# Kernel optimization log

Measured on AMD Instinct MI355X. Metric: run time of the kernel, lower is better.

The kernel has to match this reference:

```python
import jax, jax.numpy as jnp
import numpy as np

jax.config.update("jax_enable_x64", True)  # torch casts to double for matrix_exp

EPS_DIAG = 1e-6


def setup_inputs() -> dict:
    key = jax.random.key(0)
    B, D, NB, S = 32, 128, 8, 128
    ks = jax.random.split(key, 9)
    return {
        "z0r": jax.random.normal(ks[0], (B, D), jnp.float32),
        "z0i": jax.random.normal(ks[1], (B, D), jnp.float32),
        # uniform grid: dt = time_steps[0] = 0.01, diffs == dt (uniform branch)
        "time_steps": (jnp.arange(S, dtype=jnp.float32) + 1.0) * 0.01,
        "k_coeffs": jax.random.normal(ks[2], (B, NB), jnp.float32),
        "r_coeffs": jax.random.normal(ks[3], (B, NB), jnp.float32),
        "alpha": jax.random.normal(ks[4], (B, 1), jnp.float32),
        "beta": jax.random.normal(ks[5], (B, 1), jnp.float32),
        "K_bases": jax.random.normal(ks[6], (NB, D, D), jnp.float32) * 0.01,
        "R_bases": jax.random.normal(ks[7], (NB, D, D), jnp.float32) * 0.01,
    }


def _build_generator(k_coeffs, r_coeffs, alpha, beta, K_bases, R_bases):
    # A = alpha * skew(K_sum) + beta * -(R_sum^T @ R_sum), per batch element
    K_sum = jnp.einsum("bn,nij->bij", k_coeffs, K_bases)
    R_sum = jnp.einsum("bn,nij->bij", r_coeffs, R_bases)
    skew = K_sum - jnp.swapaxes(K_sum, -1, -2)
    neg_gram = -jnp.einsum("bji,bjk->bik", R_sum, R_sum)  # -(R^T @ R)
    return alpha[..., None] * skew + beta[..., None] * neg_gram  # (B, D, D)


def _propagators(A, time_steps, uniform):
    D = A.shape[-1]
    S = time_steps.shape[0]
    if uniform:
        dt = time_steps[0]
        A64 = A.astype(jnp.float64) * dt.astype(jnp.float64) + EPS_DIAG * jnp.eye(D, dtype=jnp.float64)
        M = jax.vmap(jax.scipy.linalg.expm)(A64).astype(jnp.complex64)  # (B, D, D)
        # cumulative matrix powers M, M^2, ..., M^S via O(log S) associative scan
        Ms = jnp.broadcast_to(M[:, None], (M.shape[0], S, D, D))
        props = jax.lax.associative_scan(jnp.matmul, Ms, axis=1)
    else:
        A_t = A[:, None].astype(jnp.float64) * time_steps.astype(jnp.float64)[None, :, None, None]
        props = jax.vmap(jax.vmap(jax.scipy.linalg.expm))(A_t).astype(jnp.complex64)
    return props  # (B, S, D, D)


def reference(z0r, z0i, time_steps, k_coeffs, r_coeffs, alpha, beta, K_bases, R_bases):
    ts = np.asarray(time_steps)
    uniform = ts.shape[0] <= 1 or np.allclose(ts[1:] - ts[:-1], ts[0], atol=1e-6)
    A = _build_generator(k_coeffs, r_coeffs, alpha, beta, K_bases, R_bases)
    props = _propagators(A, time_steps, uniform)
    z = (z0r + 1j * z0i).astype(jnp.complex64)  # (B, D)
    # z_evolved[b, s, o] = sum_i z[b, i] * props[b, s, o, i]
    return jnp.einsum("bi,bsoi->bso", z, props)
```

## Files before the change

kernel.cpp:

```cpp
#include <hip/hip_runtime.h>

#define BATCH   32
#define DIM     128
#define NBASES  8
#define SSTEPS  128
#define LDA     136

typedef __attribute__((ext_vector_type(8))) short s8v;
typedef __attribute__((ext_vector_type(4))) short s4v;
typedef __attribute__((ext_vector_type(4))) float f4v;

__device__ __forceinline__ f4v mf(s8v a, s8v b, f4v c) {
    return __builtin_amdgcn_mfma_f32_16x16x32_bf16(a, b, c, 0, 0, 0);
}
__device__ __forceinline__ s8v ld8(const short* p) {
    return *reinterpret_cast<const s8v*>(p);
}
__device__ __forceinline__ s4v ld4(const short* p) {
    return *reinterpret_cast<const s4v*>(p);
}
__device__ __forceinline__ void st4(short* p, s4v v) {
    *reinterpret_cast<s4v*>(p) = v;
}
__device__ __forceinline__ float upbf(short h) {
    return __uint_as_float(((unsigned)(unsigned short)h) << 16);
}
__device__ __forceinline__ void splitbf(float v, short& hi, short& lo) {
    const unsigned u = __float_as_uint(v);
    hi = (short)(u >> 16);
    const float fh = __uint_as_float(u & 0xffff0000u);
    lo = (short)(__float_as_uint(v - fh) >> 16);
}

__device__ __forceinline__ void write_out(float* __restrict__ outF, int b, int sidx,
                                          int o, int c, float val,
                                          int interleaved, int out_size)
{
    if (interleaved) {
        const int oi = ((b * SSTEPS + sidx) * DIM + o) * 2 + c;
        if (oi < out_size) outF[oi] = val;
    } else if (c == 0) {
        const int oi = (b * SSTEPS + sidx) * DIM + o;
        if (oi < out_size) outF[oi] = val;
    }
}

template<bool DUAL>
__device__ __forceinline__ void mm_full(const short* __restrict__ Ah,
                                        const short* __restrict__ Al,
                                        const short* __restrict__ Bh,
                                        const short* __restrict__ Bl,
                                        f4v acc[2][2], f4v acct[2][2],
                                        int mb, int nb, int lane)
{
    const int l15 = lane & 15, quad = lane >> 4;
    #pragma unroll
    for (int kk = 0; kk < DIM; kk += 32) {
        const int ko = kk + quad * 8;
        s8v ah[2], al[2], bh[2], bl[2];
        #pragma unroll
        for (int i = 0; i < 2; ++i) {
            ah[i] = ld8(Ah + (mb + i * 16 + l15) * LDA + ko);
            al[i] = ld8(Al + (mb + i * 16 + l15) * LDA + ko);
            bh[i] = ld8(Bh + (nb + i * 16 + l15) * LDA + ko);
            bl[i] = ld8(Bl + (nb + i * 16 + l15) * LDA + ko);
        }
        #pragma unroll
        for (int mi = 0; mi < 2; ++mi)
            #pragma unroll
            for (int ni = 0; ni < 2; ++ni) {
                acc[mi][ni] = mf(ah[mi], bh[ni], acc[mi][ni]);
                acc[mi][ni] = mf(ah[mi], bl[ni], acc[mi][ni]);
                acc[mi][ni] = mf(al[mi], bh[ni], acc[mi][ni]);
                if (DUAL) {
                    acct[ni][mi] = mf(bh[ni], ah[mi], acct[ni][mi]);
                    acct[ni][mi] = mf(bl[ni], ah[mi], acct[ni][mi]);
                    acct[ni][mi] = mf(bh[ni], al[mi], acct[ni][mi]);
                }
            }
    }
}

__global__ __launch_bounds__(1024) __attribute__((amdgpu_waves_per_eu(4, 4)))
void htg_mfma(const float* __restrict__ z0r, const float* __restrict__ z0i,
              const float* __restrict__ ts,  const float* __restrict__ kco,
              const float* __restrict__ rco, const float* __restrict__ alp,
              const float* __restrict__ bet, const float* __restrict__ KB,
              const float* __restrict__ RB,  float* __restrict__ outF,
              int interleaved, int out_size)
{
    __shared__ short nm_hi[DIM * LDA], nm_lo[DIM * LDA];
    __shared__ short tr_hi[DIM * LDA], tr_lo[DIM * LDA];
    __shared__ short ht_hi[32 * LDA],  ht_lo[32 * LDA];
    float* s_part = reinterpret_cast<float*>(nm_hi);

    const int b = blockIdx.x, t = threadIdx.x;
    const int w = t >> 6, lane = t & 63;
    const int l15 = lane & 15, quad = lane >> 4;
    const f4v z4 = {0.f, 0.f, 0.f, 0.f};
    const int mb = (w & 3) * 32, nb = (w >> 2) * 32;

    {
        float rc[NBASES], kc[NBASES];
        #pragma unroll
        for (int n = 0; n < NBASES; ++n) {
            rc[n] = rco[b * NBASES + n];
            kc[n] = kco[b * NBASES + n];
        }
        #pragma unroll
        for (int q = 0; q < 4; ++q) {
            const int e = q * 4096 + t * 4;
            float4 r4 = {0.f, 0.f, 0.f, 0.f}, k4 = {0.f, 0.f, 0.f, 0.f};
            #pragma unroll
            for (int n = 0; n < NBASES; ++n) {
                const float4 rv = *reinterpret_cast<const float4*>(RB + n * DIM * DIM + e);
                const float4 kv = *reinterpret_cast<const float4*>(KB + n * DIM * DIM + e);
                r4.x += rc[n] * rv.x; r4.y += rc[n] * rv.y;
                r4.z += rc[n] * rv.z; r4.w += rc[n] * rv.w;
                k4.x += kc[n] * kv.x; k4.y += kc[n] * kv.y;
                k4.z += kc[n] * kv.z; k4.w += kc[n] * kv.w;
            }
            const int r = e >> 7, c = e & 127;
            const float rr[4] = {r4.x, r4.y, r4.z, r4.w};
            const float kk[4] = {k4.x, k4.y, k4.z, k4.w};
            s4v kh, kl;
            #pragma unroll
            for (int j = 0; j < 4; ++j) {
                short hi, lo;
                splitbf(rr[j], hi, lo);
                tr_hi[(c + j) * LDA + r] = hi; tr_lo[(c + j) * LDA + r] = lo;
                splitbf(kk[j], hi, lo);
                kh[j] = hi; kl[j] = lo;
            }
            st4(&nm_hi[r * LDA + c], kh);
            st4(&nm_lo[r * LDA + c], kl);
        }
        if (t < 2 * DIM) {
            const int c = t >> 7, o = t & 127;
            const float zv = (c == 0) ? z0r[b * DIM + o] : z0i[b * DIM + o];
            short hi, lo; splitbf(zv, hi, lo);
            ht_hi[c * LDA + o] = hi; ht_lo[c * LDA + o] = lo;
        }
    }
    __syncthreads();

    f4v acc[2][2], acct[2][2];
    float xsave[2][2][4];

    #pragma unroll
    for (int i = 0; i < 2; ++i)
        #pragma unroll
        for (int j = 0; j < 2; ++j) acc[i][j] = z4;
    mm_full<false>(tr_hi, tr_lo, tr_hi, tr_lo, acc, acct, mb, nb, lane);
    __syncthreads();
    {
        const float alpha = alp[b], beta = bet[b], dtf = ts[0];
        #pragma unroll
        for (int mi = 0; mi < 2; ++mi)
            #pragma unroll
            for (int ni = 0; ni < 2; ++ni) {
                const int row0 = mb + mi * 16 + quad * 4;
                const int col  = nb + ni * 16 + l15;
                const s4v k2h = ld4(&nm_hi[col * LDA + row0]);
                const s4v k2l = ld4(&nm_lo[col * LDA + row0]);
                #pragma unroll
                for (int r = 0; r < 4; ++r) {
                    const int row = row0 + r;
                    const float k1 = upbf(nm_hi[row * LDA + col]) + upbf(nm_lo[row * LDA + col]);
                    const float k2 = upbf(k2h[r]) + upbf(k2l[r]);
                    float x = (alpha * (k1 - k2) - beta * acc[mi][ni][r]) * dtf;
                    if (row == col) x += 1e-6f;
                    acc[mi][ni][r] = x;
                    xsave[mi][ni][r] = x;
                }
            }
    }
    __syncthreads();
    #pragma unroll
    for (int mi = 0; mi < 2; ++mi)
        #pragma unroll
        for (int ni = 0; ni < 2; ++ni) {
            const int row0 = mb + mi * 16 + quad * 4;
            const int col  = nb + ni * 16 + l15;
            s4v h4, l4;
            #pragma unroll
            for (int r = 0; r < 4; ++r) {
                short hi, lo;
                splitbf(acc[mi][ni][r], hi, lo);
                nm_hi[(row0 + r) * LDA + col] = hi;
                nm_lo[(row0 + r) * LDA + col] = lo;
                h4[r] = hi; l4[r] = lo;
            }
            st4(&tr_hi[col * LDA + row0], h4);
            st4(&tr_lo[col * LDA + row0], l4);
        }
    __syncthreads();

    #pragma unroll
    for (int i = 0; i < 2; ++i)
        #pragma unroll
        for (int j = 0; j < 2; ++j) { acc[i][j] = z4; acct[i][j] = z4; }
    mm_full<true>(nm_hi, nm_lo, tr_hi, tr_lo, acc, acct, mb, nb, lane);
    __syncthreads();
    #pragma unroll
    for (int mi = 0; mi < 2; ++mi)
        #pragma unroll
        for (int ni = 0; ni < 2; ++ni) {
            const int row0 = mb + mi * 16 + quad * 4;
            const int col  = nb + ni * 16 + l15;
            s4v h4, l4;
            #pragma unroll
            for (int r = 0; r < 4; ++r) {
                const int row = row0 + r;
                const float xv = xsave[mi][ni][r];
                const float cv = acc[mi][ni][r];
                const float a2 = xv * (1.f / 6.f) + cv * (1.f / 24.f);
                xsave[mi][ni][r] = ((row == col) ? 1.f : 0.f) + xv + 0.5f * cv;
                short hi, lo;
                splitbf(a2, hi, lo);
                h4[r] = hi; l4[r] = lo;
            }
            st4(&tr_hi[col * LDA + row0], h4);
            st4(&tr_lo[col * LDA + row0], l4);
        }
    #pragma unroll
    for (int ti = 0; ti < 2; ++ti)
        #pragma unroll
        for (int tj = 0; tj < 2; ++tj) {
            const int rt0 = nb + ti * 16 + quad * 4;
            const int ct  = mb + tj * 16 + l15;
            s4v h4, l4;
            #pragma unroll
            for (int r = 0; r < 4; ++r) {
                short hi, lo;
                splitbf(acct[ti][tj][r], hi, lo);
                h4[r] = hi; l4[r] = lo;
            }
            st4(&nm_hi[ct * LDA + rt0], h4);
            st4(&nm_lo[ct * LDA + rt0], l4);
        }
    __syncthreads();

    #pragma unroll
    for (int mi = 0; mi < 2; ++mi)
        #pragma unroll
        for (int ni = 0; ni < 2; ++ni)
            #pragma unroll
            for (int r = 0; r < 4; ++r) acc[mi][ni][r] = xsave[mi][ni][r];
    mm_full<false>(nm_hi, nm_lo, tr_hi, tr_lo, acc, acct, mb, nb, lane);
    __syncthreads();
    #pragma unroll
    for (int mi = 0; mi < 2; ++mi)
        #pragma unroll
        for (int ni = 0; ni < 2; ++ni) {
            const int row0 = mb + mi * 16 + quad * 4;
            const int col  = nb + ni * 16 + l15;
            s4v h4, l4;
            #pragma unroll
            for (int r = 0; r < 4; ++r) {
                short hi, lo;
                splitbf(acc[mi][ni][r], hi, lo);
                nm_hi[(row0 + r) * LDA + col] = hi;
                nm_lo[(row0 + r) * LDA + col] = lo;
                h4[r] = hi; l4[r] = lo;
            }
            st4(&tr_hi[col * LDA + row0], h4);
            st4(&tr_lo[col * LDA + row0], l4);
        }
    __syncthreads();

    #pragma unroll
    for (int stage = 0; stage < 4; ++stage) {
        const int J = 1 << stage;
        f4v ar = z4;
        #pragma unroll
        for (int i = 0; i < 2; ++i)
            #pragma unroll
            for (int j = 0; j < 2; ++j) { acc[i][j] = z4; acct[i][j] = z4; }
        if (w < 8) {
            #pragma unroll
            for (int kk = 0; kk < DIM; kk += 32) {
                const int ko = kk + quad * 8;
                const s8v rah = ld8(nm_hi + (w * 16 + l15) * LDA + ko);
                const s8v ral = ld8(nm_lo + (w * 16 + l15) * LDA + ko);
                const s8v rbh = ld8(ht_hi + l15 * LDA + ko);
                const s8v rbl = ld8(ht_lo + l15 * LDA + ko);
                ar = mf(rah, rbh, ar);
                ar = mf(rah, rbl, ar);
                ar = mf(ral, rbh, ar);
            }
        }
        mm_full<true>(nm_hi, nm_lo, tr_hi, tr_lo, acc, acct, mb, nb, lane);
        __syncthreads();
        if (w < 8 && l15 < 2 * J) {
            const int o0 = w * 16 + quad * 4;
            const int sidx = (l15 >> 1) + J - 1;
            s4v h4, l4;
            #pragma unroll
            for (int r = 0; r < 4; ++r) {
                short hi, lo;
                splitbf(ar[r], hi, lo);
                h4[r] = hi; l4[r] = lo;
                write_out(outF, b, sidx, o0 + r, l15 & 1, ar[r], interleaved, out_size);
            }
            st4(&ht_hi[(l15 + 2 * J) * LDA + o0], h4);
            st4(&ht_lo[(l15 + 2 * J) * LDA + o0], l4);
        }
        #pragma unroll
        for (int mi = 0; mi < 2; ++mi)
            #pragma unroll
            for (int ni = 0; ni < 2; ++ni) {
                const int row0 = mb + mi * 16 + quad * 4;
                const int col  = nb + ni * 16 + l15;
                s4v h4, l4;
                #pragma unroll
                for (int r = 0; r < 4; ++r) {
                    short hi, lo;
                    splitbf(acc[mi][ni][r], hi, lo);
                    h4[r] = hi; l4[r] = lo;
                }
                st4(&tr_hi[col * LDA + row0], h4);
                st4(&tr_lo[col * LDA + row0], l4);
            }
        #pragma unroll
        for (int ti = 0; ti < 2; ++ti)
            #pragma unroll
            for (int tj = 0; tj < 2; ++tj) {
                const int rt0 = nb + ti * 16 + quad * 4;
                const int ct  = mb + tj * 16 + l15;
                s4v h4, l4;
                #pragma unroll
                for (int r = 0; r < 4; ++r) {
                    short hi, lo;
                    splitbf(acct[ti][tj][r], hi, lo);
                    h4[r] = hi; l4[r] = lo;
                }
                st4(&nm_hi[ct * LDA + rt0], h4);
                st4(&nm_lo[ct * LDA + rt0], l4);
            }
        __syncthreads();
    }

    const int sw = w >> 1, ct = w & 1;
    s8v vah[4], val[4];
    #pragma unroll
    for (int k4 = 0; k4 < 4; ++k4) {
        const int ko = k4 * 32 + quad * 8;
        vah[k4] = ld8(nm_hi + (sw * 16 + l15) * LDA + ko);
        val[k4] = ld8(nm_lo + (sw * 16 + l15) * LDA + ko);
    }
    for (int q = 1; q <= 7; ++q) {
        f4v a2 = z4;
        #pragma unroll
        for (int k4 = 0; k4 < 4; ++k4) {
            const int ko = k4 * 32 + quad * 8;
            const s8v bh = ld8(ht_hi + (ct * 16 + l15) * LDA + ko);
            const s8v bl = ld8(ht_lo + (ct * 16 + l15) * LDA + ko);
            a2 = mf(vah[k4], bh, a2);
            a2 = mf(vah[k4], bl, a2);
            a2 = mf(val[k4], bh, a2);
        }
        __syncthreads();
        {
            const int o0 = sw * 16 + quad * 4;
            const int n = ct * 16 + l15;
            const int sidx = 16 * q + (n >> 1) - 1;
            s4v h4, l4;
            #pragma unroll
            for (int r = 0; r < 4; ++r) {
                short hi, lo;
                splitbf(a2[r], hi, lo);
                h4[r] = hi; l4[r] = lo;
                write_out(outF, b, sidx, o0 + r, n & 1, a2[r], interleaved, out_size);
            }
            if (q < 7 || n < 2) {
                st4(&ht_hi[n * LDA + o0], h4);
                st4(&ht_lo[n * LDA + o0], l4);
            }
        }
        __syncthreads();
    }

    {
        const int o = t & 127, c = (t >> 7) & 1, kq = t >> 8;
        const int k0 = kq * 32;
        float a = 0.f;
        #pragma unroll 8
        for (int i = k0; i < k0 + 32; ++i)
            a += (upbf(tr_hi[i * LDA + o]) + upbf(tr_lo[i * LDA + o]))
               * (upbf(ht_hi[c * LDA + i]) + upbf(ht_lo[c * LDA + i]));
        s_part[t] = a;
    }
    __syncthreads();
    if (t < 2 * DIM) {
        const int o = t & 127, c = t >> 7;
        const float a = s_part[t] + s_part[t + 256] + s_part[t + 512] + s_part[t + 768];
        write_out(outF, b, 127, o, c, a, interleaved, out_size);
    }
}

extern "C" void kernel_launch(void* const* d_in, const int* in_sizes, int n_in,
                              void* d_out, int out_size, void* d_ws, size_t ws_size,
                              hipStream_t stream)
{
    (void)in_sizes; (void)n_in; (void)d_ws; (void)ws_size;
    const float* z0r = (const float*)d_in[0];
    const float* z0i = (const float*)d_in[1];
    const float* ts  = (const float*)d_in[2];
    const float* kco = (const float*)d_in[3];
    const float* rco = (const float*)d_in[4];
    const float* alp = (const float*)d_in[5];
    const float* bet = (const float*)d_in[6];
    const float* KB  = (const float*)d_in[7];
    const float* RB  = (const float*)d_in[8];
    float* outF = (float*)d_out;

    const int interleaved = (out_size >= 2 * BATCH * SSTEPS * DIM) ? 1 : 0;

    htg_mfma<<<dim3(BATCH), dim3(1024), 0, stream>>>(
        z0r, z0i, ts, kco, rco, alp, bet, KB, RB, outF, interleaved, out_size);
}
```

Baseline: 122.6 us.

## Fuse generator build with transposed product, double-buffer history, drop final reduction

The generator A is now built by computing the R^T R product and its transpose in one pass, writing both nm and tr layouts directly. This removes a separate pass and one barrier. The last squaring stage only computes the transposed product it actually needs. The sequential propagation loop now ping-pongs between two history buffers, which removes one barrier per iteration, and it runs an eighth iteration that replaces the scalar final-step reduction. The cost is more MFMA work in the first matmul and an extra loop iteration that is partly wasted.

```diff
diff --git a/kernel.cpp b/kernel.cpp
--- a/kernel.cpp
+++ b/kernel.cpp
@@ -45,7 +45,7 @@
     }
 }
 
-template<bool DUAL>
+template<bool TRO, bool NMO>
 __device__ __forceinline__ void mm_full(const short* __restrict__ Ah,
                                         const short* __restrict__ Al,
                                         const short* __restrict__ Bh,
@@ -69,10 +69,12 @@
         for (int mi = 0; mi < 2; ++mi)
             #pragma unroll
             for (int ni = 0; ni < 2; ++ni) {
-                acc[mi][ni] = mf(ah[mi], bh[ni], acc[mi][ni]);
-                acc[mi][ni] = mf(ah[mi], bl[ni], acc[mi][ni]);
-                acc[mi][ni] = mf(al[mi], bh[ni], acc[mi][ni]);
-                if (DUAL) {
+                if (TRO) {
+                    acc[mi][ni] = mf(ah[mi], bh[ni], acc[mi][ni]);
+                    acc[mi][ni] = mf(ah[mi], bl[ni], acc[mi][ni]);
+                    acc[mi][ni] = mf(al[mi], bh[ni], acc[mi][ni]);
+                }
+                if (NMO) {
                     acct[ni][mi] = mf(bh[ni], ah[mi], acct[ni][mi]);
                     acct[ni][mi] = mf(bl[ni], ah[mi], acct[ni][mi]);
                     acct[ni][mi] = mf(bh[ni], al[mi], acct[ni][mi]);
@@ -92,7 +94,6 @@
     __shared__ short nm_hi[DIM * LDA], nm_lo[DIM * LDA];
     __shared__ short tr_hi[DIM * LDA], tr_lo[DIM * LDA];
     __shared__ short ht_hi[32 * LDA],  ht_lo[32 * LDA];
-    float* s_part = reinterpret_cast<float*>(nm_hi);
 
     const int b = blockIdx.x, t = threadIdx.x;
     const int w = t >> 6, lane = t & 63;
@@ -147,60 +148,87 @@
     f4v acc[2][2], acct[2][2];
     float xsave[2][2][4];
 
-    #pragma unroll
-    for (int i = 0; i < 2; ++i)
-        #pragma unroll
-        for (int j = 0; j < 2; ++j) acc[i][j] = z4;
-    mm_full<false>(tr_hi, tr_lo, tr_hi, tr_lo, acc, acct, mb, nb, lane);
-    __syncthreads();
-    {
-        const float alpha = alp[b], beta = bet[b], dtf = ts[0];
-        #pragma unroll
-        for (int mi = 0; mi < 2; ++mi)
-            #pragma unroll
-            for (int ni = 0; ni < 2; ++ni) {
+    float kd[2][2][4], kdT[2][2][4];
+    #pragma unroll
+    for (int mi = 0; mi < 2; ++mi)
+        #pragma unroll
+        for (int ni = 0; ni < 2; ++ni) {
+            {
                 const int row0 = mb + mi * 16 + quad * 4;
                 const int col  = nb + ni * 16 + l15;
                 const s4v k2h = ld4(&nm_hi[col * LDA + row0]);
                 const s4v k2l = ld4(&nm_lo[col * LDA + row0]);
                 #pragma unroll
+                for (int r = 0; r < 4; ++r)
+                    kd[mi][ni][r] = (upbf(nm_hi[(row0 + r) * LDA + col]) +
+                                     upbf(nm_lo[(row0 + r) * LDA + col]))
+                                  - (upbf(k2h[r]) + upbf(k2l[r]));
+            }
+            {
+                const int rt0 = nb + mi * 16 + quad * 4;
+                const int ct  = mb + ni * 16 + l15;
+                const s4v k1h = ld4(&nm_hi[ct * LDA + rt0]);
+                const s4v k1l = ld4(&nm_lo[ct * LDA + rt0]);
+                #pragma unroll
+                for (int r = 0; r < 4; ++r)
+                    kdT[mi][ni][r] = (upbf(k1h[r]) + upbf(k1l[r]))
+                                   - (upbf(nm_hi[(rt0 + r) * LDA + ct]) +
+                                      upbf(nm_lo[(rt0 + r) * LDA + ct]));
+            }
+        }
+    #pragma unroll
+    for (int i = 0; i < 2; ++i)
+        #pragma unroll
+        for (int j = 0; j < 2; ++j) { acc[i][j] = z4; acct[i][j] = z4; }
+    mm_full<true, true>(tr_hi, tr_lo, tr_hi, tr_lo, acc, acct, mb, nb, lane);
+    __syncthreads();
+    {
+        const float alpha = alp[b], beta = bet[b], dtf = ts[0];
+        #pragma unroll
+        for (int mi = 0; mi < 2; ++mi)
+            #pragma unroll
+            for (int ni = 0; ni < 2; ++ni) {
+                const int row0 = mb + mi * 16 + quad * 4;
+                const int col  = nb + ni * 16 + l15;
+                s4v h4, l4;
+                #pragma unroll
                 for (int r = 0; r < 4; ++r) {
-                    const int row = row0 + r;
-                    const float k1 = upbf(nm_hi[row * LDA + col]) + upbf(nm_lo[row * LDA + col]);
-                    const float k2 = upbf(k2h[r]) + upbf(k2l[r]);
-                    float x = (alpha * (k1 - k2) - beta * acc[mi][ni][r]) * dtf;
-                    if (row == col) x += 1e-6f;
-                    acc[mi][ni][r] = x;
+                    float x = (alpha * kd[mi][ni][r] - beta * acc[mi][ni][r]) * dtf;
+                    if (row0 + r == col) x += 1e-6f;
                     xsave[mi][ni][r] = x;
-                }
-            }
-    }
-    __syncthreads();
-    #pragma unroll
-    for (int mi = 0; mi < 2; ++mi)
-        #pragma unroll
-        for (int ni = 0; ni < 2; ++ni) {
-            const int row0 = mb + mi * 16 + quad * 4;
-            const int col  = nb + ni * 16 + l15;
-            s4v h4, l4;
-            #pragma unroll
-            for (int r = 0; r < 4; ++r) {
-                short hi, lo;
-                splitbf(acc[mi][ni][r], hi, lo);
-                nm_hi[(row0 + r) * LDA + col] = hi;
-                nm_lo[(row0 + r) * LDA + col] = lo;
-                h4[r] = hi; l4[r] = lo;
-            }
-            st4(&tr_hi[col * LDA + row0], h4);
-            st4(&tr_lo[col * LDA + row0], l4);
-        }
+                    short hi, lo;
+                    splitbf(x, hi, lo);
+                    h4[r] = hi; l4[r] = lo;
+                }
+                st4(&tr_hi[col * LDA + row0], h4);
+                st4(&tr_lo[col * LDA + row0], l4);
+            }
+        #pragma unroll
+        for (int ti = 0; ti < 2; ++ti)
+            #pragma unroll
+            for (int tj = 0; tj < 2; ++tj) {
+                const int rt0 = nb + ti * 16 + quad * 4;
+                const int ct  = mb + tj * 16 + l15;
+                s4v h4, l4;
+                #pragma unroll
+                for (int r = 0; r < 4; ++r) {
+                    float x = (alpha * kdT[ti][tj][r] - beta * acct[ti][tj][r]) * dtf;
+                    if (ct == rt0 + r) x += 1e-6f;
+                    short hi, lo;
+                    splitbf(x, hi, lo);
+                    h4[r] = hi; l4[r] = lo;
+                }
+                st4(&nm_hi[ct * LDA + rt0], h4);
+                st4(&nm_lo[ct * LDA + rt0], l4);
+            }
+    }
     __syncthreads();
 
     #pragma unroll
     for (int i = 0; i < 2; ++i)
         #pragma unroll
         for (int j = 0; j < 2; ++j) { acc[i][j] = z4; acct[i][j] = z4; }
-    mm_full<true>(nm_hi, nm_lo, tr_hi, tr_lo, acc, acct, mb, nb, lane);
+    mm_full<true, true>(nm_hi, nm_lo, tr_hi, tr_lo, acc, acct, mb, nb, lane);
     __syncthreads();
     #pragma unroll
     for (int mi = 0; mi < 2; ++mi)
@@ -247,7 +275,7 @@
         for (int ni = 0; ni < 2; ++ni)
             #pragma unroll
             for (int r = 0; r < 4; ++r) acc[mi][ni][r] = xsave[mi][ni][r];
-    mm_full<false>(nm_hi, nm_lo, tr_hi, tr_lo, acc, acct, mb, nb, lane);
+    mm_full<true, false>(nm_hi, nm_lo, tr_hi, tr_lo, acc, acct, mb, nb, lane);
     __syncthreads();
     #pragma unroll
     for (int mi = 0; mi < 2; ++mi)
@@ -270,7 +298,7 @@
     __syncthreads();
 
     #pragma unroll
-    for (int stage = 0; stage < 4; ++stage) {
+    for (int stage = 0; stage < 3; ++stage) {
         const int J = 1 << stage;
         f4v ar = z4;
         #pragma unroll
@@ -290,7 +318,7 @@
                 ar = mf(ral, rbh, ar);
             }
         }
-        mm_full<true>(nm_hi, nm_lo, tr_hi, tr_lo, acc, acct, mb, nb, lane);
+        mm_full<true, true>(nm_hi, nm_lo, tr_hi, tr_lo, acc, acct, mb, nb, lane);
         __syncthreads();
         if (w < 8 && l15 < 2 * J) {
             const int o0 = w * 16 + quad * 4;
@@ -341,6 +369,61 @@
         __syncthreads();
     }
 
+    {
+        const int J = 8;
+        f4v ar = z4;
+        #pragma unroll
+        for (int i = 0; i < 2; ++i)
+            #pragma unroll
+            for (int j = 0; j < 2; ++j) acct[i][j] = z4;
+        if (w < 8) {
+            #pragma unroll
+            for (int kk = 0; kk < DIM; kk += 32) {
+                const int ko = kk + quad * 8;
+                const s8v rah = ld8(nm_hi + (w * 16 + l15) * LDA + ko);
+                const s8v ral = ld8(nm_lo + (w * 16 + l15) * LDA + ko);
+                const s8v rbh = ld8(ht_hi + l15 * LDA + ko);
+                const s8v rbl = ld8(ht_lo + l15 * LDA + ko);
+                ar = mf(rah, rbh, ar);
+                ar = mf(rah, rbl, ar);
+                ar = mf(ral, rbh, ar);
+            }
+        }
+        mm_full<false, true>(nm_hi, nm_lo, tr_hi, tr_lo, acc, acct, mb, nb, lane);
+        __syncthreads();
+        if (w < 8 && l15 < 2 * J) {
+            const int o0 = w * 16 + quad * 4;
+            const int sidx = (l15 >> 1) + J - 1;
+            s4v h4, l4;
+            #pragma unroll
+            for (int r = 0; r < 4; ++r) {
+                short hi, lo;
+                splitbf(ar[r], hi, lo);
+                h4[r] = hi; l4[r] = lo;
+                write_out(outF, b, sidx, o0 + r, l15 & 1, ar[r], interleaved, out_size);
+            }
+            st4(&ht_hi[(l15 + 2 * J) * LDA + o0], h4);
+            st4(&ht_lo[(l15 + 2 * J) * LDA + o0], l4);
+        }
+        #pragma unroll
+        for (int ti = 0; ti < 2; ++ti)
+            #pragma unroll
+            for (int tj = 0; tj < 2; ++tj) {
+                const int rt0 = nb + ti * 16 + quad * 4;
+                const int ct  = mb + tj * 16 + l15;
+                s4v h4, l4;
+                #pragma unroll
+                for (int r = 0; r < 4; ++r) {
+                    short hi, lo;
+                    splitbf(acct[ti][tj][r], hi, lo);
+                    h4[r] = hi; l4[r] = lo;
+                }
+                st4(&nm_hi[ct * LDA + rt0], h4);
+                st4(&nm_lo[ct * LDA + rt0], l4);
+            }
+        __syncthreads();
+    }
+
     const int sw = w >> 1, ct = w & 1;
     s8v vah[4], val[4];
     #pragma unroll
@@ -349,18 +432,20 @@
         vah[k4] = ld8(nm_hi + (sw * 16 + l15) * LDA + ko);
         val[k4] = ld8(nm_lo + (sw * 16 + l15) * LDA + ko);
     }
-    for (int q = 1; q <= 7; ++q) {
+    short *rh_hi = ht_hi, *rh_lo = ht_lo;
+    short *wh_hi = tr_hi, *wh_lo = tr_lo;
+    #pragma unroll
+    for (int q = 1; q <= 8; ++q) {
         f4v a2 = z4;
         #pragma unroll
         for (int k4 = 0; k4 < 4; ++k4) {
             const int ko = k4 * 32 + quad * 8;
-            const s8v bh = ld8(ht_hi + (ct * 16 + l15) * LDA + ko);
-            const s8v bl = ld8(ht_lo + (ct * 16 + l15) * LDA + ko);
+            const s8v bh = ld8(rh_hi + (ct * 16 + l15) * LDA + ko);
+            const s8v bl = ld8(rh_lo + (ct * 16 + l15) * LDA + ko);
             a2 = mf(vah[k4], bh, a2);
             a2 = mf(vah[k4], bl, a2);
             a2 = mf(val[k4], bh, a2);
         }
-        __syncthreads();
         {
             const int o0 = sw * 16 + quad * 4;
             const int n = ct * 16 + l15;
@@ -371,31 +456,18 @@
                 short hi, lo;
                 splitbf(a2[r], hi, lo);
                 h4[r] = hi; l4[r] = lo;
-                write_out(outF, b, sidx, o0 + r, n & 1, a2[r], interleaved, out_size);
-            }
-            if (q < 7 || n < 2) {
-                st4(&ht_hi[n * LDA + o0], h4);
-                st4(&ht_lo[n * LDA + o0], l4);
+                if (sidx < SSTEPS)
+                    write_out(outF, b, sidx, o0 + r, n & 1, a2[r], interleaved, out_size);
+            }
+            if (q < 8) {
+                st4(&wh_hi[n * LDA + o0], h4);
+                st4(&wh_lo[n * LDA + o0], l4);
             }
         }
         __syncthreads();
-    }
-
-    {
-        const int o = t & 127, c = (t >> 7) & 1, kq = t >> 8;
-        const int k0 = kq * 32;
-        float a = 0.f;
-        #pragma unroll 8
-        for (int i = k0; i < k0 + 32; ++i)
-            a += (upbf(tr_hi[i * LDA + o]) + upbf(tr_lo[i * LDA + o]))
-               * (upbf(ht_hi[c * LDA + i]) + upbf(ht_lo[c * LDA + i]));
-        s_part[t] = a;
-    }
-    __syncthreads();
-    if (t < 2 * DIM) {
-        const int o = t & 127, c = t >> 7;
-        const float a = s_part[t] + s_part[t + 256] + s_part[t + 512] + s_part[t + 768];
-        write_out(outF, b, 127, o, c, a, interleaved, out_size);
+        short* tp;
+        tp = rh_hi; rh_hi = wh_hi; wh_hi = tp;
+        tp = rh_lo; rh_lo = wh_lo; wh_lo = tp;
     }
 }
 
```

New measurement: 118.4 us. -3.4%, faster.
